# Kernel optimization log

Measured on AMD Instinct MI355X. Metric: run time of the kernel, lower is better.

Reference implementation:

```python
import jax, jax.numpy as jnp
import numpy as np

D_IN = 1024
D_OUT = 1024
SEQ = 4096


def setup_inputs() -> dict:
    key = jax.random.key(0)
    kx, kq, kk, kv = jax.random.split(key, 4)
    x = jax.random.normal(kx, (SEQ, D_IN), dtype=jnp.float32)
    # torch Linear weights: [d_out, d_in], y = x @ W.T; no bias (qkv_bias=False)
    s = 1.0 / np.sqrt(D_IN)
    Wq = jax.random.uniform(kq, (D_OUT, D_IN), dtype=jnp.float32, minval=-s, maxval=s)
    Wk = jax.random.uniform(kk, (D_OUT, D_IN), dtype=jnp.float32, minval=-s, maxval=s)
    Wv = jax.random.uniform(kv, (D_OUT, D_IN), dtype=jnp.float32, minval=-s, maxval=s)
    return {"x": x, "Wq": Wq, "Wk": Wk, "Wv": Wv}


def reference(x, Wq, Wk, Wv):
    seq = x.shape[0]
    q = x @ Wq.T  # [S, d_out]
    k = x @ Wk.T
    v = x @ Wv.T
    scores = q @ k.T  # [S, S]
    # causal mask: positions j > i masked to -inf (triu, diagonal=1)
    causal = jnp.tril(jnp.ones((seq, seq), dtype=bool))
    scores = jnp.where(causal, scores, -jnp.inf)
    attn = jax.nn.softmax(scores / jnp.sqrt(jnp.float32(q.shape[-1])), axis=-1)
    return attn @ v  # [S, d_out]
```

## Files before the change

kernel.cpp:

```cpp
#include <hip/hip_runtime.h>
#include <hip/hip_bf16.h>
#include <cstdint>
#include <cstddef>


#define SEQQ 4096
#define DDIM 1024

typedef __bf16 bf16x8 __attribute__((ext_vector_type(8)));
typedef float f32x4 __attribute__((ext_vector_type(4)));

__device__ __forceinline__ unsigned short f2bf(float f) {
  unsigned int u = __builtin_bit_cast(unsigned int, f);
  unsigned int r = u + 0x7FFFu + ((u >> 16) & 1u);
  return (unsigned short)(r >> 16);
}

__device__ __forceinline__ float bf2f(unsigned short b) {
  return __builtin_bit_cast(float, (unsigned int)b << 16);
}

__device__ __forceinline__ void gload_lds16(const void* g, void* lds) {
  __builtin_amdgcn_global_load_lds(
      (__attribute__((address_space(1))) void*)(uintptr_t)g,
      (__attribute__((address_space(3))) void*)(uintptr_t)lds, 16, 0, 0);
}

__global__ __launch_bounds__(256) void cvt_all(const float* __restrict__ x,
                                               const float* __restrict__ Wq,
                                               const float* __restrict__ Wk,
                                               const float* __restrict__ Wv,
                                               unsigned short* __restrict__ xb,
                                               unsigned short* __restrict__ Wcat) {
  int b = blockIdx.x;
  const float* src;
  unsigned short* dst;
  float scale = 1.0f;
  if (b < 4096) {
    src = x; dst = xb;
  } else if (b < 5120) {
    src = Wq; dst = Wcat; scale = 0.03125f; b -= 4096;
  } else if (b < 6144) {
    src = Wk; dst = Wcat + (1u << 20); b -= 5120;
  } else {
    src = Wv; dst = Wcat + (2u << 20); b -= 6144;
  }
  const int i = (b * 256 + threadIdx.x) * 4;
  const float4 v = *reinterpret_cast<const float4*>(src + i);
  ushort4 o;
  o.x = f2bf(v.x * scale);
  o.y = f2bf(v.y * scale);
  o.z = f2bf(v.z * scale);
  o.w = f2bf(v.w * scale);
  *reinterpret_cast<ushort4*>(dst + i) = o;
}

#define GEMM_PRE()                                                          \
  __shared__ unsigned short As[3][8192] __attribute__((aligned(16)));       \
  __shared__ unsigned short Bs[3][8192] __attribute__((aligned(16)));       \
  const int tid = threadIdx.x;                                              \
  const int wave = tid >> 6, lane = tid & 63;                               \
  const int wr = (wave >> 2) * 128, wc = (wave & 3) * 64;                   \
  f32x4 acc[8][4] = {};                                                     \
  int offA[8], offB[4];                                                     \
  {                                                                         \
    const int cb = (lane >> 4) * 16;                                        \
    const int rA = wr + (lane & 15);                                        \
    _Pragma("unroll")                                                       \
    for (int m = 0; m < 8; ++m) {                                           \
      int o = (rA + m * 16) * 64 + cb;                                      \
      offA[m] = o ^ (((o >> 9) & 1) << 5);                                  \
    }                                                                       \
    const int rB = wc + (lane & 15);                                        \
    _Pragma("unroll")                                                       \
    for (int n = 0; n < 4; ++n) {                                           \
      int o = (rB + n * 16) * 64 + cb;                                      \
      offB[n] = o ^ (((o >> 9) & 1) << 5);                                  \
    }                                                                       \
  }

#define GEMM_LOOP(ABASE, LDA, BBASE, LDB, S0, S1)                           \
  do {                                                                      \
    const int nt = (S1) - (S0);                                             \
    const char *pA0, *pA1, *pB0, *pB1;                                      \
    {                                                                       \
      const size_t srow = wave * 16 + (lane >> 2);                          \
      const int scb = ((lane & 3) * 16) ^ (((lane >> 5) & 1) << 5);         \
      pA0 = (const char*)(ABASE) + srow * ((size_t)(LDA) * 2) +             \
            (size_t)(S0) * 64 + scb;                                        \
      pA1 = pA0 + (size_t)128 * ((size_t)(LDA) * 2);                        \
      pB0 = (const char*)(BBASE) + srow * ((size_t)(LDB) * 2) +             \
            (size_t)(S0) * 64 + scb;                                        \
      pB1 = pB0 + (size_t)128 * ((size_t)(LDB) * 2);                        \
    }                                                                       \
    char* ldsA = (char*)&As[0][0];                                          \
    char* ldsB = (char*)&Bs[0][0];                                          \
    const int wofs = wave * 1024;                                           \
    gload_lds16(pA0, ldsA + wofs);                                          \
    gload_lds16(pA1, ldsA + 8192 + wofs);                                   \
    gload_lds16(pB0, ldsB + wofs);                                          \
    gload_lds16(pB1, ldsB + 8192 + wofs);                                   \
    pA0 += 64; pA1 += 64; pB0 += 64; pB1 += 64;                             \
    if (nt > 1) {                                                           \
      gload_lds16(pA0, ldsA + 16384 + wofs);                                \
      gload_lds16(pA1, ldsA + 16384 + 8192 + wofs);                         \
      gload_lds16(pB0, ldsB + 16384 + wofs);                                \
      gload_lds16(pB1, ldsB + 16384 + 8192 + wofs);                         \
      pA0 += 64; pA1 += 64; pB0 += 64; pB1 += 64;                           \
      asm volatile("s_waitcnt vmcnt(4)" ::: "memory");                      \
    } else {                                                                \
      asm volatile("s_waitcnt vmcnt(0)" ::: "memory");                      \
    }                                                                       \
    asm volatile("s_barrier" ::: "memory");                                 \
    int rb = 0;                                                             \
    for (int s = 0; s < nt; ++s) {                                          \
      const int bofs = rb * 16384;                                          \
      bf16x8 a[8], b[4];                                                    \
      _Pragma("unroll")                                                     \
      for (int m = 0; m < 8; ++m)                                           \
        a[m] = *(const bf16x8*)(ldsA + bofs + offA[m]);                     \
      _Pragma("unroll")                                                     \
      for (int n = 0; n < 4; ++n)                                           \
        b[n] = *(const bf16x8*)(ldsB + bofs + offB[n]);                     \
      if (s + 2 < nt) {                                                     \
        const int wofs2 = ((rb >= 1) ? rb - 1 : 2) * 16384 + wofs;          \
        gload_lds16(pA0, ldsA + wofs2);                                     \
        gload_lds16(pA1, ldsA + wofs2 + 8192);                              \
        gload_lds16(pB0, ldsB + wofs2);                                     \
        gload_lds16(pB1, ldsB + wofs2 + 8192);                              \
        pA0 += 64; pA1 += 64; pB0 += 64; pB1 += 64;                         \
        asm volatile("s_waitcnt lgkmcnt(0)" ::: "memory");                  \
        asm volatile("s_waitcnt vmcnt(4)" ::: "memory");                    \
      } else if (s + 1 < nt) {                                              \
        asm volatile("s_waitcnt lgkmcnt(0)" ::: "memory");                  \
        asm volatile("s_waitcnt vmcnt(0)" ::: "memory");                    \
      } else {                                                              \
        asm volatile("s_waitcnt lgkmcnt(0)" ::: "memory");                  \
      }                                                                     \
      asm volatile("s_barrier" ::: "memory");                               \
      __builtin_amdgcn_s_setprio(1);                                        \
      _Pragma("unroll")                                                     \
      for (int m = 0; m < 8; ++m)                                           \
        _Pragma("unroll")                                                   \
        for (int n = 0; n < 4; ++n)                                         \
          acc[m][n] = __builtin_amdgcn_mfma_f32_16x16x32_bf16(              \
              a[m], b[n], acc[m][n], 0, 0, 0);                              \
      __builtin_amdgcn_s_setprio(0);                                        \
      rb = (rb == 2) ? 0 : rb + 1;                                          \
    }                                                                       \
  } while (0)

__device__ __forceinline__ int xcd_swz(int id, int n) {
  return (id & 7) * (n >> 3) + (id >> 3);
}

__global__ __launch_bounds__(512, 1) void gemm_qkv(const unsigned short* __restrict__ X,
                                                   const unsigned short* __restrict__ W,
                                                   unsigned short* __restrict__ Qb,
                                                   unsigned short* __restrict__ Kb,
                                                   unsigned short* __restrict__ Vt) {
  const int id = xcd_swz(blockIdx.x, 192);
  const int by = id / 12, bx = id - by * 12;
  GEMM_PRE();
  const int brow = by * 256, bcol = bx * 256;
  GEMM_LOOP(X + (size_t)brow * DDIM, DDIM, W + (size_t)bcol * DDIM, DDIM, 0, 32);
  const int region = bcol >> 10;
  const int lcol = bcol & 1023;
  const int c0 = wc + (lane & 15);
  const int r0 = wr + ((lane >> 4) << 2);
  if (region < 2) {
    unsigned short* dst = (region == 0) ? Qb : Kb;
#pragma unroll
    for (int m = 0; m < 8; ++m) {
      const int r = brow + r0 + m * 16;
#pragma unroll
      for (int n = 0; n < 4; ++n) {
        const int c = lcol + c0 + n * 16;
#pragma unroll
        for (int j = 0; j < 4; ++j)
          dst[(size_t)(r + j) * DDIM + c] = f2bf(acc[m][n][j]);
      }
    }
  } else {
#pragma unroll
    for (int m = 0; m < 8; ++m) {
      const int r = brow + r0 + m * 16;
#pragma unroll
      for (int n = 0; n < 4; ++n) {
        const int c = lcol + c0 + n * 16;
        ushort4 pk;
        pk.x = f2bf(acc[m][n][0]);
        pk.y = f2bf(acc[m][n][1]);
        pk.z = f2bf(acc[m][n][2]);
        pk.w = f2bf(acc[m][n][3]);
        *reinterpret_cast<ushort4*>(Vt + (size_t)c * SEQQ + r) = pk;
      }
    }
  }
}

__global__ __launch_bounds__(512, 1) void gemm_qkt(const unsigned short* __restrict__ Qb,
                                                   const unsigned short* __restrict__ Kb,
                                                   unsigned short* __restrict__ S,
                                                   float* __restrict__ tsw) {
  const int id = xcd_swz(blockIdx.x, 136);
  int bi = (int)((sqrtf(8.0f * (float)id + 1.0f) - 1.0f) * 0.5f);
  while ((bi + 1) * (bi + 2) / 2 <= id) ++bi;
  while (bi * (bi + 1) / 2 > id) --bi;
  const int bj = id - bi * (bi + 1) / 2;
  GEMM_PRE();
  const int brow = bi * 256, bcol = bj * 256;
  GEMM_LOOP(Qb + (size_t)brow * DDIM, DDIM, Kb + (size_t)bcol * DDIM, DDIM, 0, 32);
  const int c0 = wc + (lane & 15);
  const int r0 = wr + ((lane >> 4) << 2);
  float* tswp = tsw + ((size_t)id * 4 + (wave & 3)) * 256;
#pragma unroll
  for (int m = 0; m < 8; ++m) {
    const int r = brow + r0 + m * 16;
    float rs[4] = {0.f, 0.f, 0.f, 0.f};
#pragma unroll
    for (int n = 0; n < 4; ++n) {
      const int c = bcol + c0 + n * 16;
#pragma unroll
      for (int j = 0; j < 4; ++j) {
        const float e = (c > r + j) ? 0.0f : __expf(acc[m][n][j]);
        rs[j] += e;
        S[(size_t)(r + j) * SEQQ + c] = (c > r + j) ? (unsigned short)0
                                                    : f2bf(e);
      }
    }
#pragma unroll
    for (int j = 0; j < 4; ++j) {
#pragma unroll
      for (int o = 8; o; o >>= 1) rs[j] += __shfl_xor(rs[j], o);
    }
    if ((lane & 15) == 0) {
#pragma unroll
      for (int j = 0; j < 4; ++j) tswp[r0 + m * 16 + j] = rs[j];
    }
  }
}

__device__ __forceinline__ int pv_nc(int bi) { return (8 * bi + 29) / 22; }

__global__ __launch_bounds__(512, 1) void gemm_pv_split(const unsigned short* __restrict__ P,
                                                        const unsigned short* __restrict__ Vt,
                                                        const float* __restrict__ tsw,
                                                        float* __restrict__ O,
                                                        unsigned short* __restrict__ partB) {
  const int t = blockIdx.x >> 2, bj = blockIdx.x & 3;
  int bi = 0, pre = 0;
  while (pre + pv_nc(bi) <= t) { pre += pv_nc(bi); ++bi; }
  const int ck = t - pre;
  const int nc = pv_nc(bi);
  const int kt = (bi + 1) * 8;
  const int W = (kt + nc - 1) / nc;
  const int s0 = ck * W;
  const int s1 = min(s0 + W, kt);

  GEMM_PRE();
  __shared__ float rinv[256];
  if (tid < 256) {
    const int t0 = bi * (bi + 1) / 2;
    float s = 0.f;
    for (int tt = t0; tt <= t0 + bi; ++tt) {
#pragma unroll
      for (int w = 0; w < 4; ++w) s += tsw[((size_t)tt * 4 + w) * 256 + tid];
    }
    rinv[tid] = 1.0f / s;
  }
  __syncthreads();

  const int brow = bi * 256, bcol = bj * 256;
  GEMM_LOOP(P + (size_t)brow * SEQQ, SEQQ, Vt + (size_t)bcol * SEQQ, SEQQ, s0, s1);
  const int c0 = wc + (lane & 15);
  const int r0 = wr + ((lane >> 4) << 2);
  if (bi < 2) {
#pragma unroll
    for (int m = 0; m < 8; ++m) {
      const int lr = r0 + m * 16;
      const int r = brow + lr;
#pragma unroll
      for (int j = 0; j < 4; ++j) {
        const float ri = rinv[lr + j];
#pragma unroll
        for (int n = 0; n < 4; ++n) {
          const int c = bcol + c0 + n * 16;
          O[(size_t)(r + j) * DDIM + c] = acc[m][n][j] * ri;
        }
      }
    }
  } else {
    unsigned short* tile = partB + ((size_t)(pre - 2 + ck) * 4 + bj) * 65536;
#pragma unroll
    for (int m = 0; m < 8; ++m) {
      const int lr = r0 + m * 16;
#pragma unroll
      for (int j = 0; j < 4; ++j) {
        const float ri = rinv[lr + j];
#pragma unroll
        for (int n = 0; n < 4; ++n) {
          const int lc = c0 + n * 16;
          tile[(lr + j) * 256 + lc] = f2bf(acc[m][n][j] * ri);
        }
      }
    }
  }
}

__global__ __launch_bounds__(256) void reduce_pv(float* __restrict__ O,
                                                 const unsigned short* __restrict__ partB) {
  const int idx = blockIdx.x * 256 + threadIdx.x;
  const int r = 512 + (idx >> 8);
  const int cc = (idx & 255) * 4;
  const int bi = r >> 8;
  const int nc = pv_nc(bi);
  int sb = 0;
  for (int b = 0; b < bi; ++b) sb += pv_nc(b);
  sb -= 2;
  const int bj = cc >> 8;
  const int lr = r & 255, lc = cc & 255;
  float4 a = make_float4(0.f, 0.f, 0.f, 0.f);
  for (int k = 0; k < nc; ++k) {
    const ushort4 p = *reinterpret_cast<const ushort4*>(
        partB + ((size_t)(sb + k) * 4 + bj) * 65536 + lr * 256 + lc);
    a.x += bf2f(p.x); a.y += bf2f(p.y); a.z += bf2f(p.z); a.w += bf2f(p.w);
  }
  *reinterpret_cast<float4*>(O + (size_t)r * DDIM + cc) = a;
}

extern "C" void kernel_launch(void* const* d_in, const int* in_sizes, int n_in,
                              void* d_out, int out_size, void* d_ws, size_t ws_size,
                              hipStream_t stream) {
  (void)in_sizes; (void)n_in; (void)out_size; (void)ws_size;
  const float* x = (const float*)d_in[0];
  const float* Wq = (const float*)d_in[1];
  const float* Wk = (const float*)d_in[2];
  const float* Wv = (const float*)d_in[3];
  float* out = (float*)d_out;

  char* ws = (char*)d_ws;
  unsigned short* xb   = (unsigned short*)(ws);
  unsigned short* Wcat = (unsigned short*)(ws + ((size_t)8 << 20));
  unsigned short* Qb   = (unsigned short*)(ws + ((size_t)14 << 20));
  unsigned short* Kb   = (unsigned short*)(ws + ((size_t)22 << 20));
  unsigned short* Vt   = (unsigned short*)(ws + ((size_t)30 << 20));
  unsigned short* S    = (unsigned short*)(ws + ((size_t)38 << 20));
  float* tsw            = (float*)ws;
  unsigned short* partB = (unsigned short*)(ws + ((size_t)2 << 20));

  cvt_all<<<7168, 256, 0, stream>>>(x, Wq, Wk, Wv, xb, Wcat);
  gemm_qkv<<<192, 512, 0, stream>>>(xb, Wcat, Qb, Kb, Vt);
  gemm_qkt<<<136, 512, 0, stream>>>(Qb, Kb, S, tsw);
  gemm_pv_split<<<228, 512, 0, stream>>>(S, Vt, tsw, out, partB);
  reduce_pv<<<3584, 256, 0, stream>>>(out, partB);
}
```

Measured before the change: 118.6 us.

## Fuse all five stages into one cooperative persistent kernel with grid syncs

```diff
diff --git a/kernel.cpp b/kernel.cpp
--- a/kernel.cpp
+++ b/kernel.cpp
@@ -1,11 +1,14 @@
 #include <hip/hip_runtime.h>
 #include <hip/hip_bf16.h>
+#include <hip/hip_cooperative_groups.h>
 #include <cstdint>
 #include <cstddef>
 
 
 #define SEQQ 4096
 #define DDIM 1024
+
+namespace cg = cooperative_groups;
 
 typedef __bf16 bf16x8 __attribute__((ext_vector_type(8)));
 typedef float f32x4 __attribute__((ext_vector_type(4)));
@@ -26,38 +29,13 @@
       (__attribute__((address_space(3))) void*)(uintptr_t)lds, 16, 0, 0);
 }
 
-__global__ __launch_bounds__(256) void cvt_all(const float* __restrict__ x,
-                                               const float* __restrict__ Wq,
-                                               const float* __restrict__ Wk,
-                                               const float* __restrict__ Wv,
-                                               unsigned short* __restrict__ xb,
-                                               unsigned short* __restrict__ Wcat) {
-  int b = blockIdx.x;
-  const float* src;
-  unsigned short* dst;
-  float scale = 1.0f;
-  if (b < 4096) {
-    src = x; dst = xb;
-  } else if (b < 5120) {
-    src = Wq; dst = Wcat; scale = 0.03125f; b -= 4096;
-  } else if (b < 6144) {
-    src = Wk; dst = Wcat + (1u << 20); b -= 5120;
-  } else {
-    src = Wv; dst = Wcat + (2u << 20); b -= 6144;
-  }
-  const int i = (b * 256 + threadIdx.x) * 4;
-  const float4 v = *reinterpret_cast<const float4*>(src + i);
-  ushort4 o;
-  o.x = f2bf(v.x * scale);
-  o.y = f2bf(v.y * scale);
-  o.z = f2bf(v.z * scale);
-  o.w = f2bf(v.w * scale);
-  *reinterpret_cast<ushort4*>(dst + i) = o;
-}
-
-#define GEMM_PRE()                                                          \
-  __shared__ unsigned short As[3][8192] __attribute__((aligned(16)));       \
-  __shared__ unsigned short Bs[3][8192] __attribute__((aligned(16)));       \
+__device__ __forceinline__ int xcd_swz(int id, int n) {
+  return (id & 7) * (n >> 3) + (id >> 3);
+}
+
+__device__ __forceinline__ int pv_nc(int bi) { return (8 * bi + 29) / 22; }
+
+#define GEMM_REGS()                                                         \
   const int tid = threadIdx.x;                                              \
   const int wave = tid >> 6, lane = tid & 63;                               \
   const int wr = (wave >> 2) * 128, wc = (wave & 3) * 64;                   \
@@ -150,183 +128,202 @@
     }                                                                       \
   } while (0)
 
-__device__ __forceinline__ int xcd_swz(int id, int n) {
-  return (id & 7) * (n >> 3) + (id >> 3);
-}
-
-__global__ __launch_bounds__(512, 1) void gemm_qkv(const unsigned short* __restrict__ X,
-                                                   const unsigned short* __restrict__ W,
-                                                   unsigned short* __restrict__ Qb,
-                                                   unsigned short* __restrict__ Kb,
-                                                   unsigned short* __restrict__ Vt) {
-  const int id = xcd_swz(blockIdx.x, 192);
-  const int by = id / 12, bx = id - by * 12;
-  GEMM_PRE();
-  const int brow = by * 256, bcol = bx * 256;
-  GEMM_LOOP(X + (size_t)brow * DDIM, DDIM, W + (size_t)bcol * DDIM, DDIM, 0, 32);
-  const int region = bcol >> 10;
-  const int lcol = bcol & 1023;
-  const int c0 = wc + (lane & 15);
-  const int r0 = wr + ((lane >> 4) << 2);
-  if (region < 2) {
-    unsigned short* dst = (region == 0) ? Qb : Kb;
+__global__ __launch_bounds__(512, 1) void fused_all(
+    const float* __restrict__ x, const float* __restrict__ Wq,
+    const float* __restrict__ Wk, const float* __restrict__ Wv,
+    unsigned short* __restrict__ xb, unsigned short* __restrict__ Wcat,
+    unsigned short* __restrict__ Qb, unsigned short* __restrict__ Kb,
+    unsigned short* __restrict__ Vt, unsigned short* __restrict__ S,
+    float* __restrict__ tsw, float* __restrict__ O,
+    unsigned short* __restrict__ partB) {
+  __shared__ unsigned short As[3][8192] __attribute__((aligned(16)));
+  __shared__ unsigned short Bs[3][8192] __attribute__((aligned(16)));
+  __shared__ float rinvS[256];
+  cg::grid_group grid = cg::this_grid();
+  const int bid = blockIdx.x;
+  const int th = threadIdx.x;
+
+  for (int gid = bid * 512 + th; gid < 1835008; gid += 131072) {
+    const float* src;
+    unsigned short* dst;
+    float scale = 1.0f;
+    int e;
+    if (gid < 1048576)      { src = x;  dst = xb;             e = gid; }
+    else if (gid < 1310720) { src = Wq; dst = Wcat;           e = gid - 1048576; scale = 0.03125f; }
+    else if (gid < 1572864) { src = Wk; dst = Wcat + (1u<<20); e = gid - 1310720; }
+    else                    { src = Wv; dst = Wcat + (2u<<20); e = gid - 1572864; }
+    const int i = e * 4;
+    const float4 v = *reinterpret_cast<const float4*>(src + i);
+    ushort4 o;
+    o.x = f2bf(v.x * scale);
+    o.y = f2bf(v.y * scale);
+    o.z = f2bf(v.z * scale);
+    o.w = f2bf(v.w * scale);
+    *reinterpret_cast<ushort4*>(dst + i) = o;
+  }
+  grid.sync();
+
+  if (bid < 192) {
+    const int id = xcd_swz(bid, 192);
+    const int by = id / 12, bx = id - by * 12;
+    GEMM_REGS();
+    const int brow = by * 256, bcol = bx * 256;
+    GEMM_LOOP(xb + (size_t)brow * DDIM, DDIM, Wcat + (size_t)bcol * DDIM, DDIM, 0, 32);
+    const int region = bcol >> 10;
+    const int lcol = bcol & 1023;
+    const int c0 = wc + (lane & 15);
+    const int r0 = wr + ((lane >> 4) << 2);
+    if (region < 2) {
+      unsigned short* dst = (region == 0) ? Qb : Kb;
+#pragma unroll
+      for (int m = 0; m < 8; ++m) {
+        const int r = brow + r0 + m * 16;
+#pragma unroll
+        for (int n = 0; n < 4; ++n) {
+          const int c = lcol + c0 + n * 16;
+#pragma unroll
+          for (int j = 0; j < 4; ++j)
+            dst[(size_t)(r + j) * DDIM + c] = f2bf(acc[m][n][j]);
+        }
+      }
+    } else {
+#pragma unroll
+      for (int m = 0; m < 8; ++m) {
+        const int r = brow + r0 + m * 16;
+#pragma unroll
+        for (int n = 0; n < 4; ++n) {
+          const int c = lcol + c0 + n * 16;
+          ushort4 pk;
+          pk.x = f2bf(acc[m][n][0]);
+          pk.y = f2bf(acc[m][n][1]);
+          pk.z = f2bf(acc[m][n][2]);
+          pk.w = f2bf(acc[m][n][3]);
+          *reinterpret_cast<ushort4*>(Vt + (size_t)c * SEQQ + r) = pk;
+        }
+      }
+    }
+  }
+  grid.sync();
+
+  if (bid < 136) {
+    const int id = xcd_swz(bid, 136);
+    int bi = (int)((sqrtf(8.0f * (float)id + 1.0f) - 1.0f) * 0.5f);
+    while ((bi + 1) * (bi + 2) / 2 <= id) ++bi;
+    while (bi * (bi + 1) / 2 > id) --bi;
+    const int bj = id - bi * (bi + 1) / 2;
+    GEMM_REGS();
+    const int brow = bi * 256, bcol = bj * 256;
+    GEMM_LOOP(Qb + (size_t)brow * DDIM, DDIM, Kb + (size_t)bcol * DDIM, DDIM, 0, 32);
+    const int c0 = wc + (lane & 15);
+    const int r0 = wr + ((lane >> 4) << 2);
+    float* tswp = tsw + ((size_t)id * 4 + (wave & 3)) * 256;
 #pragma unroll
     for (int m = 0; m < 8; ++m) {
       const int r = brow + r0 + m * 16;
+      float rs[4] = {0.f, 0.f, 0.f, 0.f};
 #pragma unroll
       for (int n = 0; n < 4; ++n) {
-        const int c = lcol + c0 + n * 16;
-#pragma unroll
-        for (int j = 0; j < 4; ++j)
-          dst[(size_t)(r + j) * DDIM + c] = f2bf(acc[m][n][j]);
-      }
-    }
-  } else {
-#pragma unroll
-    for (int m = 0; m < 8; ++m) {
-      const int r = brow + r0 + m * 16;
-#pragma unroll
-      for (int n = 0; n < 4; ++n) {
-        const int c = lcol + c0 + n * 16;
-        ushort4 pk;
-        pk.x = f2bf(acc[m][n][0]);
-        pk.y = f2bf(acc[m][n][1]);
-        pk.z = f2bf(acc[m][n][2]);
-        pk.w = f2bf(acc[m][n][3]);
-        *reinterpret_cast<ushort4*>(Vt + (size_t)c * SEQQ + r) = pk;
-      }
-    }
-  }
-}
-
-__global__ __launch_bounds__(512, 1) void gemm_qkt(const unsigned short* __restrict__ Qb,
-                                                   const unsigned short* __restrict__ Kb,
-                                                   unsigned short* __restrict__ S,
-                                                   float* __restrict__ tsw) {
-  const int id = xcd_swz(blockIdx.x, 136);
-  int bi = (int)((sqrtf(8.0f * (float)id + 1.0f) - 1.0f) * 0.5f);
-  while ((bi + 1) * (bi + 2) / 2 <= id) ++bi;
-  while (bi * (bi + 1) / 2 > id) --bi;
-  const int bj = id - bi * (bi + 1) / 2;
-  GEMM_PRE();
-  const int brow = bi * 256, bcol = bj * 256;
-  GEMM_LOOP(Qb + (size_t)brow * DDIM, DDIM, Kb + (size_t)bcol * DDIM, DDIM, 0, 32);
-  const int c0 = wc + (lane & 15);
-  const int r0 = wr + ((lane >> 4) << 2);
-  float* tswp = tsw + ((size_t)id * 4 + (wave & 3)) * 256;
-#pragma unroll
-  for (int m = 0; m < 8; ++m) {
-    const int r = brow + r0 + m * 16;
-    float rs[4] = {0.f, 0.f, 0.f, 0.f};
-#pragma unroll
-    for (int n = 0; n < 4; ++n) {
-      const int c = bcol + c0 + n * 16;
+        const int c = bcol + c0 + n * 16;
+#pragma unroll
+        for (int j = 0; j < 4; ++j) {
+          const float e = (c > r + j) ? 0.0f : __expf(acc[m][n][j]);
+          rs[j] += e;
+          S[(size_t)(r + j) * SEQQ + c] = (c > r + j) ? (unsigned short)0
+                                                      : f2bf(e);
+        }
+      }
 #pragma unroll
       for (int j = 0; j < 4; ++j) {
-        const float e = (c > r + j) ? 0.0f : __expf(acc[m][n][j]);
-        rs[j] += e;
-        S[(size_t)(r + j) * SEQQ + c] = (c > r + j) ? (unsigned short)0
-                                                    : f2bf(e);
-      }
-    }
-#pragma unroll
-    for (int j = 0; j < 4; ++j) {
-#pragma unroll
-      for (int o = 8; o; o >>= 1) rs[j] += __shfl_xor(rs[j], o);
-    }
-    if ((lane & 15) == 0) {
-#pragma unroll
-      for (int j = 0; j < 4; ++j) tswp[r0 + m * 16 + j] = rs[j];
-    }
-  }
-}
-
-__device__ __forceinline__ int pv_nc(int bi) { return (8 * bi + 29) / 22; }
-
-__global__ __launch_bounds__(512, 1) void gemm_pv_split(const unsigned short* __restrict__ P,
-                                                        const unsigned short* __restrict__ Vt,
-                                                        const float* __restrict__ tsw,
-                                                        float* __restrict__ O,
-                                                        unsigned short* __restrict__ partB) {
-  const int t = blockIdx.x >> 2, bj = blockIdx.x & 3;
-  int bi = 0, pre = 0;
-  while (pre + pv_nc(bi) <= t) { pre += pv_nc(bi); ++bi; }
-  const int ck = t - pre;
-  const int nc = pv_nc(bi);
-  const int kt = (bi + 1) * 8;
-  const int W = (kt + nc - 1) / nc;
-  const int s0 = ck * W;
-  const int s1 = min(s0 + W, kt);
-
-  GEMM_PRE();
-  __shared__ float rinv[256];
-  if (tid < 256) {
-    const int t0 = bi * (bi + 1) / 2;
-    float s = 0.f;
-    for (int tt = t0; tt <= t0 + bi; ++tt) {
-#pragma unroll
-      for (int w = 0; w < 4; ++w) s += tsw[((size_t)tt * 4 + w) * 256 + tid];
-    }
-    rinv[tid] = 1.0f / s;
-  }
-  __syncthreads();
-
-  const int brow = bi * 256, bcol = bj * 256;
-  GEMM_LOOP(P + (size_t)brow * SEQQ, SEQQ, Vt + (size_t)bcol * SEQQ, SEQQ, s0, s1);
-  const int c0 = wc + (lane & 15);
-  const int r0 = wr + ((lane >> 4) << 2);
-  if (bi < 2) {
-#pragma unroll
-    for (int m = 0; m < 8; ++m) {
-      const int lr = r0 + m * 16;
-      const int r = brow + lr;
-#pragma unroll
-      for (int j = 0; j < 4; ++j) {
-        const float ri = rinv[lr + j];
-#pragma unroll
-        for (int n = 0; n < 4; ++n) {
-          const int c = bcol + c0 + n * 16;
-          O[(size_t)(r + j) * DDIM + c] = acc[m][n][j] * ri;
-        }
-      }
-    }
-  } else {
-    unsigned short* tile = partB + ((size_t)(pre - 2 + ck) * 4 + bj) * 65536;
-#pragma unroll
-    for (int m = 0; m < 8; ++m) {
-      const int lr = r0 + m * 16;
-#pragma unroll
-      for (int j = 0; j < 4; ++j) {
-        const float ri = rinv[lr + j];
-#pragma unroll
-        for (int n = 0; n < 4; ++n) {
-          const int lc = c0 + n * 16;
-          tile[(lr + j) * 256 + lc] = f2bf(acc[m][n][j] * ri);
-        }
-      }
-    }
-  }
-}
-
-__global__ __launch_bounds__(256) void reduce_pv(float* __restrict__ O,
-                                                 const unsigned short* __restrict__ partB) {
-  const int idx = blockIdx.x * 256 + threadIdx.x;
-  const int r = 512 + (idx >> 8);
-  const int cc = (idx & 255) * 4;
-  const int bi = r >> 8;
-  const int nc = pv_nc(bi);
-  int sb = 0;
-  for (int b = 0; b < bi; ++b) sb += pv_nc(b);
-  sb -= 2;
-  const int bj = cc >> 8;
-  const int lr = r & 255, lc = cc & 255;
-  float4 a = make_float4(0.f, 0.f, 0.f, 0.f);
-  for (int k = 0; k < nc; ++k) {
-    const ushort4 p = *reinterpret_cast<const ushort4*>(
-        partB + ((size_t)(sb + k) * 4 + bj) * 65536 + lr * 256 + lc);
-    a.x += bf2f(p.x); a.y += bf2f(p.y); a.z += bf2f(p.z); a.w += bf2f(p.w);
-  }
-  *reinterpret_cast<float4*>(O + (size_t)r * DDIM + cc) = a;
+#pragma unroll
+        for (int o = 8; o; o >>= 1) rs[j] += __shfl_xor(rs[j], o);
+      }
+      if ((lane & 15) == 0) {
+#pragma unroll
+        for (int j = 0; j < 4; ++j) tswp[r0 + m * 16 + j] = rs[j];
+      }
+    }
+  }
+  grid.sync();
+
+  if (bid < 228) {
+    const int t = bid >> 2, bj = bid & 3;
+    int bi = 0, pre = 0;
+    while (pre + pv_nc(bi) <= t) { pre += pv_nc(bi); ++bi; }
+    const int ck = t - pre;
+    const int nc = pv_nc(bi);
+    const int kt = (bi + 1) * 8;
+    const int W = (kt + nc - 1) / nc;
+    const int s0 = ck * W;
+    const int s1 = min(s0 + W, kt);
+
+    GEMM_REGS();
+    if (tid < 256) {
+      const int t0 = bi * (bi + 1) / 2;
+      float s = 0.f;
+      for (int tt = t0; tt <= t0 + bi; ++tt) {
+#pragma unroll
+        for (int w = 0; w < 4; ++w) s += tsw[((size_t)tt * 4 + w) * 256 + tid];
+      }
+      rinvS[tid] = 1.0f / s;
+    }
+    __syncthreads();
+
+    const int brow = bi * 256, bcol = bj * 256;
+    GEMM_LOOP(S + (size_t)brow * SEQQ, SEQQ, Vt + (size_t)bcol * SEQQ, SEQQ, s0, s1);
+    const int c0 = wc + (lane & 15);
+    const int r0 = wr + ((lane >> 4) << 2);
+    if (bi < 2) {
+#pragma unroll
+      for (int m = 0; m < 8; ++m) {
+        const int lr = r0 + m * 16;
+        const int r = brow + lr;
+#pragma unroll
+        for (int j = 0; j < 4; ++j) {
+          const float ri = rinvS[lr + j];
+#pragma unroll
+          for (int n = 0; n < 4; ++n) {
+            const int c = bcol + c0 + n * 16;
+            O[(size_t)(r + j) * DDIM + c] = acc[m][n][j] * ri;
+          }
+        }
+      }
+    } else {
+      unsigned short* tile = partB + ((size_t)(pre - 2 + ck) * 4 + bj) * 65536;
+#pragma unroll
+      for (int m = 0; m < 8; ++m) {
+        const int lr = r0 + m * 16;
+#pragma unroll
+        for (int j = 0; j < 4; ++j) {
+          const float ri = rinvS[lr + j];
+#pragma unroll
+          for (int n = 0; n < 4; ++n) {
+            const int lc = c0 + n * 16;
+            tile[(lr + j) * 256 + lc] = f2bf(acc[m][n][j] * ri);
+          }
+        }
+      }
+    }
+  }
+  grid.sync();
+
+  for (int idx = bid * 512 + th; idx < 917504; idx += 131072) {
+    const int r = 512 + (idx >> 8);
+    const int cc = (idx & 255) * 4;
+    const int bi = r >> 8;
+    const int nc = pv_nc(bi);
+    int sb = 0;
+    for (int b = 0; b < bi; ++b) sb += pv_nc(b);
+    sb -= 2;
+    const int bj = cc >> 8;
+    const int lr = r & 255, lc = cc & 255;
+    float4 a = make_float4(0.f, 0.f, 0.f, 0.f);
+    for (int k = 0; k < nc; ++k) {
+      const ushort4 p = *reinterpret_cast<const ushort4*>(
+          partB + ((size_t)(sb + k) * 4 + bj) * 65536 + lr * 256 + lc);
+      a.x += bf2f(p.x); a.y += bf2f(p.y); a.z += bf2f(p.z); a.w += bf2f(p.w);
+    }
+    *reinterpret_cast<float4*>(O + (size_t)r * DDIM + cc) = a;
+  }
 }
 
 extern "C" void kernel_launch(void* const* d_in, const int* in_sizes, int n_in,
@@ -340,18 +337,20 @@
   float* out = (float*)d_out;
 
   char* ws = (char*)d_ws;
-  unsigned short* xb   = (unsigned short*)(ws);
-  unsigned short* Wcat = (unsigned short*)(ws + ((size_t)8 << 20));
+  unsigned short* xb   = (unsigned short*)(ws + ((size_t)46 << 20));
+  unsigned short* Wcat = (unsigned short*)(ws + ((size_t)54 << 20));
   unsigned short* Qb   = (unsigned short*)(ws + ((size_t)14 << 20));
   unsigned short* Kb   = (unsigned short*)(ws + ((size_t)22 << 20));
   unsigned short* Vt   = (unsigned short*)(ws + ((size_t)30 << 20));
-  unsigned short* S    = (unsigned short*)(ws + ((size_t)38 << 20));
+  unsigned short* S    = (unsigned short*)(ws + ((size_t)60 << 20));
   float* tsw            = (float*)ws;
   unsigned short* partB = (unsigned short*)(ws + ((size_t)2 << 20));
 
-  cvt_all<<<7168, 256, 0, stream>>>(x, Wq, Wk, Wv, xb, Wcat);
-  gemm_qkv<<<192, 512, 0, stream>>>(xb, Wcat, Qb, Kb, Vt);
-  gemm_qkt<<<136, 512, 0, stream>>>(Qb, Kb, S, tsw);
-  gemm_pv_split<<<228, 512, 0, stream>>>(S, Vt, tsw, out, partB);
-  reduce_pv<<<3584, 256, 0, stream>>>(out, partB);
-}
+
+  void* args[] = {(void*)&x,  (void*)&Wq,  (void*)&Wk,  (void*)&Wv,
+                  (void*)&xb, (void*)&Wcat, (void*)&Qb, (void*)&Kb,
+                  (void*)&Vt, (void*)&S,   (void*)&tsw, (void*)&out,
+                  (void*)&partB};
+  hipLaunchCooperativeKernel((const void*)fused_all, dim3(256), dim3(512),
+                             args, 0, stream);
+}
```

Result: slower. 252.8 us (+113.2%).
